# Kernel tuning notes

Measured on AMD Instinct MI355X. Metric: run time of the kernel, lower is better.

The kernel has to match this reference:

```python
import jax, jax.numpy as jnp
import numpy as np

B, T, C, H, HS = 4, 2048, 1024, 16, 64
EPS = 1e-5


def setup_inputs() -> dict:
    key = jax.random.key(0)
    ks = jax.random.split(key, 16)
    s = lambda k, shp, fan: jax.random.normal(k, shp, jnp.float32) * (fan ** -0.5)
    return {
        "x": jax.random.normal(ks[0], (B, T, C), jnp.float32),
        "wq": s(ks[1], (H, C, HS), C), "bq": jnp.zeros((H, HS), jnp.float32),
        "wk": s(ks[2], (H, C, HS), C), "bk": jnp.zeros((H, HS), jnp.float32),
        "wv": s(ks[3], (H, C, HS), C), "bv": jnp.zeros((H, HS), jnp.float32),
        "wp": s(ks[4], (C, C), C), "bp": jnp.zeros((C,), jnp.float32),
        "w1": s(ks[5], (C, 4 * C), C), "b1": jnp.zeros((4 * C,), jnp.float32),
        "w2": s(ks[6], (4 * C, C), 4 * C), "b2": jnp.zeros((C,), jnp.float32),
        "g1": jnp.ones((C,), jnp.float32), "be1": jnp.zeros((C,), jnp.float32),
        "g2": jnp.ones((C,), jnp.float32), "be2": jnp.zeros((C,), jnp.float32),
    }


def _layernorm(x, g, b):
    mu = jnp.mean(x, axis=-1, keepdims=True)
    var = jnp.mean(jnp.square(x - mu), axis=-1, keepdims=True)
    return (x - mu) * jax.lax.rsqrt(var + EPS) * g + b


def reference(x, wq, bq, wk, bk, wv, bv, wp, bp, w1, b1, w2, b2, g1, be1, g2, be2):
    Bc, Tc, Cc = x.shape
    h = _layernorm(x, g1, be1)
    # per-head projections stacked: [B,H,T,HS]
    q = jnp.einsum('btc,hcd->bhtd', h, wq) + bq[None, :, None, :]
    k = jnp.einsum('btc,hcd->bhtd', h, wk) + bk[None, :, None, :]
    v = jnp.einsum('btc,hcd->bhtd', h, wv) + bv[None, :, None, :]
    # NOTE: source scales by 1/sqrt(n_embd), not 1/sqrt(head_size)
    scores = jnp.einsum('bhtd,bhsd->bhts', q, k) * (Cc ** -0.5)
    causal = jnp.tril(jnp.ones((Tc, Tc), bool))
    scores = jnp.where(causal, scores, -jnp.inf)
    attn = jax.nn.softmax(scores, axis=-1)
    out = jnp.einsum('bhts,bhsd->bhtd', attn, v)
    out = out.transpose(0, 2, 1, 3).reshape(Bc, Tc, Cc)  # concat heads
    x = x + out @ wp + bp
    h2 = _layernorm(x, g2, be2)
    ffn = jax.nn.relu(h2 @ w1 + b1) @ w2 + b2
    return x + ffn
```

## Files before the change

kernel.cpp:

```cpp
#include <hip/hip_runtime.h>


constexpr int Bb = 4, Tt = 2048, Cc = 1024, Hh = 16, HSz = 64, Ff = 4096;
constexpr int Mrows = Bb * Tt;

typedef __attribute__((ext_vector_type(8))) short bf16x8;
typedef __attribute__((ext_vector_type(4))) float f32x4;

__device__ __forceinline__ ushort f2bf(float f) {
  uint u = __builtin_bit_cast(uint, f);
  uint r = (u + 0x7fffu + ((u >> 16) & 1u)) >> 16;
  return (ushort)r;
}
__device__ __forceinline__ float bf2f(ushort s) {
  return __builtin_bit_cast(float, ((uint)s) << 16);
}
__device__ __forceinline__ uint cvtpk_bf16(float lo, float hi) {
  uint r;
  asm("v_cvt_pk_bf16_f32 %0, %1, %2" : "=v"(r) : "v"(lo), "v"(hi));
  return r;
}
__device__ __forceinline__ void gload16(const void* g, void* l) {
  __builtin_amdgcn_global_load_lds(
      (const __attribute__((address_space(1))) void*)g,
      (__attribute__((address_space(3))) void*)l, 16, 0, 0);
}

__global__ __launch_bounds__(256) void ln_kernel(const float* __restrict__ x,
                                                 const float* __restrict__ g,
                                                 const float* __restrict__ b,
                                                 ushort* __restrict__ out) {
  int row = blockIdx.x;
  const float* xr = x + (size_t)row * Cc;
  int c4 = threadIdx.x * 4;
  float4 v = *(const float4*)(xr + c4);
  float s1 = v.x + v.y + v.z + v.w;
  float s2 = v.x * v.x + v.y * v.y + v.z * v.z + v.w * v.w;
#pragma unroll
  for (int off = 32; off >= 1; off >>= 1) {
    s1 += __shfl_xor(s1, off);
    s2 += __shfl_xor(s2, off);
  }
  __shared__ float red[8];
  int wid = threadIdx.x >> 6, lane = threadIdx.x & 63;
  if (lane == 0) { red[wid] = s1; red[4 + wid] = s2; }
  __syncthreads();
  float t1 = red[0] + red[1] + red[2] + red[3];
  float t2 = red[4] + red[5] + red[6] + red[7];
  float mu = t1 * (1.0f / Cc);
  float var = t2 * (1.0f / Cc) - mu * mu;
  float rs = rsqrtf(var + 1e-5f);
  float4 gv = *(const float4*)(g + c4);
  float4 bv = *(const float4*)(b + c4);
  ushort4 o;
  o.x = f2bf((v.x - mu) * rs * gv.x + bv.x);
  o.y = f2bf((v.y - mu) * rs * gv.y + bv.y);
  o.z = f2bf((v.z - mu) * rs * gv.z + bv.z);
  o.w = f2bf((v.w - mu) * rs * gv.w + bv.w);
  *(ushort4*)(out + (size_t)row * Cc + c4) = o;
}

__device__ __forceinline__ void tcast_body(const float* __restrict__ src,
                                           ushort* __restrict__ dst, int ldS,
                                           int ldD, int r0, int c0) {
  __shared__ float t[32][33];
  int c = threadIdx.x & 31, r8 = threadIdx.x >> 5;
#pragma unroll
  for (int i = 0; i < 4; ++i) {
    int r = r8 + i * 8;
    t[r][c] = src[(size_t)(r0 + r) * ldS + c0 + c];
  }
  __syncthreads();
#pragma unroll
  for (int i = 0; i < 4; ++i) {
    int rr = r8 + i * 8;
    dst[(size_t)(c0 + rr) * ldD + r0 + c] = f2bf(t[c][rr]);
  }
}

__global__ __launch_bounds__(256) void tcast_kernel(const float* __restrict__ src,
                                                    ushort* __restrict__ dst,
                                                    int ldS, int ldD) {
  tcast_body(src, dst, ldS, ldD, blockIdx.x * 32, blockIdx.y * 32);
}

__global__ __launch_bounds__(256) void tcast_qkv(const float* __restrict__ wq,
                                                 const float* __restrict__ wk,
                                                 const float* __restrict__ wv,
                                                 ushort* __restrict__ dst) {
  int z = blockIdx.z, zz = z >> 4, h = z & 15;
  const float* src = (zz == 0 ? wq : (zz == 1 ? wk : wv)) + (size_t)h * Cc * HSz;
  ushort* d = dst + (size_t)(zz * 1024 + h * 64) * 1024;
  tcast_body(src, d, HSz, Cc, blockIdx.x * 32, blockIdx.y * 32);
}

__global__ __launch_bounds__(256) void bias_concat(const float* __restrict__ bq,
                                                   const float* __restrict__ bk,
                                                   const float* __restrict__ bv,
                                                   float* __restrict__ dst) {
  int i = blockIdx.x * 256 + threadIdx.x;
  dst[i] = i < 1024 ? bq[i] : (i < 2048 ? bk[i - 1024] : bv[i - 2048]);
}

__device__ __forceinline__ void gemm_main(const ushort* __restrict__ A, int lda,
                                          const ushort* __restrict__ Bt, int ldb,
                                          int K, int m0, int n0,
                                          ushort* __restrict__ As,
                                          ushort* __restrict__ Bs,
                                          f32x4 (&acc)[4][2]) {
  int tid = threadIdx.x, wid = tid >> 6, lane = tid & 63;
  int wr = wid >> 2, wc = wid & 3, fr = lane & 15, fq = lane >> 4;
  const ushort* Ag = A + (size_t)m0 * lda;
  const ushort* Bg = Bt + (size_t)n0 * ldb;
  for (int k0 = 0; k0 < K; k0 += 64) {
#pragma unroll
    for (int c = 0; c < 2; ++c) {
      int slot = c * 512 + tid;
      int row = slot >> 3, s = slot & 7;
      int sw = (s << 3) ^ ((row & 7) << 3);
      gload16(Ag + (size_t)row * lda + k0 + sw, As + (size_t)(c * 512 + wid * 64) * 8);
      gload16(Bg + (size_t)row * ldb + k0 + sw, Bs + (size_t)(c * 512 + wid * 64) * 8);
    }
    __syncthreads();
    bf16x8 av[4][2], bv[2][2];
#pragma unroll
    for (int m = 0; m < 4; ++m) {
      int row = wr * 64 + m * 16 + fr;
#pragma unroll
      for (int ks = 0; ks < 2; ++ks)
        av[m][ks] = *(const bf16x8*)&As[row * 64 + (((ks * 4 + fq) ^ (row & 7)) << 3)];
    }
#pragma unroll
    for (int n = 0; n < 2; ++n) {
      int row = wc * 32 + n * 16 + fr;
#pragma unroll
      for (int ks = 0; ks < 2; ++ks)
        bv[n][ks] = *(const bf16x8*)&Bs[row * 64 + (((ks * 4 + fq) ^ (row & 7)) << 3)];
    }
#pragma unroll
    for (int m = 0; m < 4; ++m)
#pragma unroll
      for (int n = 0; n < 2; ++n)
#pragma unroll
        for (int ks = 0; ks < 2; ++ks)
          acc[m][n] = __builtin_amdgcn_mfma_f32_16x16x32_bf16(
              av[m][ks], bv[n][ks], acc[m][n], 0, 0, 0);
    __syncthreads();
  }
}

__device__ __forceinline__ void xcd_swz(int& bx, int& by) {
  int bid = blockIdx.x + blockIdx.y * gridDim.x;
  int cpx = (gridDim.x * gridDim.y) >> 3;
  int id = (bid & 7) * cpx + (bid >> 3);
  bx = id % gridDim.x;
  by = id / gridDim.x;
}

template <bool RELU, bool HASRES, bool OUTBF16>
__global__ __launch_bounds__(512) void gemm_bf16(
    const ushort* __restrict__ A, int lda, const ushort* __restrict__ Bt,
    int ldb, const float* __restrict__ bias, const float* __restrict__ res,
    void* __restrict__ Cout, int ldc, int K) {
  __shared__ __align__(16) ushort As[128 * 64];
  __shared__ __align__(16) ushort Bs[128 * 64];
  f32x4 acc[4][2] = {};
  int bx, by;
  xcd_swz(bx, by);
  int m0 = by * 128, n0 = bx * 128;
  gemm_main(A, lda, Bt, ldb, K, m0, n0, As, Bs, acc);
  int lane = threadIdx.x & 63, wid = threadIdx.x >> 6;
  int wr = wid >> 2, wc = wid & 3, fr = lane & 15, fq = lane >> 4;
#pragma unroll
  for (int m = 0; m < 4; ++m) {
    int gm = m0 + wr * 64 + m * 16 + fq * 4;
#pragma unroll
    for (int n = 0; n < 2; ++n) {
      int gn = n0 + wc * 32 + n * 16 + fr;
      float bsv = bias[gn];
#pragma unroll
      for (int j = 0; j < 4; ++j) {
        int row = gm + j;
        float v = acc[m][n][j] + bsv;
        if constexpr (HASRES) v += res[(size_t)row * ldc + gn];
        if constexpr (RELU) v = fmaxf(v, 0.f);
        if constexpr (OUTBF16)
          ((ushort*)Cout)[(size_t)row * ldc + gn] = f2bf(v);
        else
          ((float*)Cout)[(size_t)row * ldc + gn] = v;
      }
    }
  }
}

__global__ __launch_bounds__(512) void gemm_qkv(const ushort* __restrict__ A,
                                                const ushort* __restrict__ Bt,
                                                const float* __restrict__ bias,
                                                ushort* __restrict__ q,
                                                ushort* __restrict__ k,
                                                ushort* __restrict__ vt) {
  __shared__ __align__(16) ushort As[128 * 64];
  __shared__ __align__(16) ushort Bs[128 * 64];
  f32x4 acc[4][2] = {};
  int bx, by;
  xcd_swz(bx, by);
  int m0 = by * 128, n0 = bx * 128;
  gemm_main(A, 1024, Bt, 1024, 1024, m0, n0, As, Bs, acc);
  int lane = threadIdx.x & 63, wid = threadIdx.x >> 6;
  int wr = wid >> 2, wc = wid & 3, fr = lane & 15, fq = lane >> 4;
  const float qscale = 1.4426950408889634f / 32.0f;
#pragma unroll
  for (int m = 0; m < 4; ++m) {
    int gm = m0 + wr * 64 + m * 16 + fq * 4;
#pragma unroll
    for (int n = 0; n < 2; ++n) {
      int gn = n0 + wc * 32 + n * 16 + fr;
      float bsv = bias[gn];
      if (gn < 1024) {
#pragma unroll
        for (int j = 0; j < 4; ++j)
          q[(size_t)(gm + j) * 1024 + gn] = f2bf((acc[m][n][j] + bsv) * qscale);
      } else if (gn < 2048) {
        int col = gn - 1024;
#pragma unroll
        for (int j = 0; j < 4; ++j)
          k[(size_t)(gm + j) * 1024 + col] = f2bf(acc[m][n][j] + bsv);
      } else {
        int dd = gn - 2048, h = dd >> 6, d = dd & 63;
        int bbr = gm >> 11, t = gm & 2047;
        ushort4 pw = {f2bf(acc[m][n][0] + bsv), f2bf(acc[m][n][1] + bsv),
                      f2bf(acc[m][n][2] + bsv), f2bf(acc[m][n][3] + bsv)};
        *(ushort4*)&vt[(((size_t)(bbr * 16 + h)) * 64 + d) * 2048 + t] = pw;
      }
    }
  }
}

constexpr int QB = 128, KVB = 64;
__global__ __launch_bounds__(512) void attn_kernel(const ushort* __restrict__ Qb,
                                                   const ushort* __restrict__ Kb,
                                                   const ushort* __restrict__ Vt,
                                                   ushort* __restrict__ att) {
  __shared__ __align__(16) ushort Klds[64 * 64];
  __shared__ __align__(16) ushort Vlds[64 * 64];
  __shared__ __align__(16) ushort Plds[8][16 * 64];
  int tid = threadIdx.x, wid = tid >> 6, lane = tid & 63;
  int fr = lane & 15, fq = lane >> 4;
  int bh = blockIdx.y, bb = bh >> 4, hh = bh & 15;
  const ushort* qkbase = Qb + ((size_t)bb * Tt) * Cc + hh * HSz;
  const ushort* Kbase = Kb + ((size_t)bb * Tt) * Cc + hh * HSz;
  const ushort* Vbase = Vt + ((size_t)(bb * Hh + hh)) * HSz * Tt;

#pragma unroll 1
  for (int pass = 0; pass < 2; ++pass) {
    int qt = pass ? (Tt / QB - 1 - (int)blockIdx.x) : (int)blockIdx.x;
    int q0 = qt * QB;
    int q0w = q0 + wid * 16;

    bf16x8 Qreg[2];
#pragma unroll
    for (int d2 = 0; d2 < 2; ++d2)
      Qreg[d2] = *(const bf16x8*)(qkbase + (size_t)(q0w + fr) * Cc + d2 * 32 + fq * 8);
    f32x4 Oa[4] = {};
    float mrow = -1e30f, lrow = 0.f;
    int nt = q0 / KVB + 2;

    for (int kt = 0; kt < nt; ++kt) {
      int t0 = kt * KVB;
      __syncthreads();
      {
        int row = tid >> 3;
        int b = (tid & 7) * 16;
        int sw = (b >> 1) ^ ((row & 7) << 3);
        gload16(Kbase + (size_t)(t0 + row) * Cc + sw, (char*)Klds + wid * 1024);
        gload16(Vbase + (size_t)row * Tt + t0 + sw, (char*)Vlds + wid * 1024);
      }
      __syncthreads();
      if (q0w + 15 < t0) continue;

      bf16x8 kf[4][2];
#pragma unroll
      for (int ks = 0; ks < 4; ++ks)
#pragma unroll
        for (int d2 = 0; d2 < 2; ++d2) {
          int row = ks * 16 + fr;
          int off = (d2 * 64 + fq * 16) ^ ((row & 7) << 4);
          kf[ks][d2] = *(const bf16x8*)((const char*)Klds + row * 128 + off);
        }
      f32x4 accs[4] = {};
      __builtin_amdgcn_s_setprio(1);
#pragma unroll
      for (int ks = 0; ks < 4; ++ks) {
        accs[ks] = __builtin_amdgcn_mfma_f32_16x16x32_bf16(
            kf[ks][0], Qreg[0], accs[ks], 0, 0, 0);
        accs[ks] = __builtin_amdgcn_mfma_f32_16x16x32_bf16(
            kf[ks][1], Qreg[1], accs[ks], 0, 0, 0);
      }
      __builtin_amdgcn_s_setprio(0);

      float sv[4][4];
      float vmax = -1e30f;
      if (t0 + 63 <= q0w) {
#pragma unroll
        for (int ks = 0; ks < 4; ++ks)
#pragma unroll
          for (int j = 0; j < 4; ++j) {
            sv[ks][j] = accs[ks][j];
            vmax = fmaxf(vmax, sv[ks][j]);
          }
      } else {
        int qg = q0w + fr;
#pragma unroll
        for (int ks = 0; ks < 4; ++ks)
#pragma unroll
          for (int j = 0; j < 4; ++j) {
            int kg = t0 + ks * 16 + fq * 4 + j;
            float s = accs[ks][j];
            s = (kg <= qg) ? s : -1e30f;
            sv[ks][j] = s;
            vmax = fmaxf(vmax, s);
          }
      }
      vmax = fmaxf(vmax, __shfl_xor(vmax, 16));
      vmax = fmaxf(vmax, __shfl_xor(vmax, 32));
      float mnew = mrow;
      if (!__all(vmax <= mnew + 11.0f)) {
        mnew = fmaxf(mrow, vmax);
        float sf = exp2f(mrow - mnew);
        mrow = mnew;
        lrow *= sf;
#pragma unroll
        for (int j = 0; j < 4; ++j) {
          float sfo = __shfl(sf, fq * 4 + j);
#pragma unroll
          for (int ds = 0; ds < 4; ++ds) Oa[ds][j] *= sfo;
        }
      }
      float ls = 0.f;
      char* pbase = (char*)Plds[wid] + fr * 128;
#pragma unroll
      for (int ks = 0; ks < 4; ++ks) {
        float p0 = exp2f(sv[ks][0] - mnew);
        float p1 = exp2f(sv[ks][1] - mnew);
        float p2 = exp2f(sv[ks][2] - mnew);
        float p3 = exp2f(sv[ks][3] - mnew);
        ls += (p0 + p1) + (p2 + p3);
        uint2 pw = {cvtpk_bf16(p0, p1), cvtpk_bf16(p2, p3)};
        int off = (ks * 32 + fq * 8) ^ ((fr & 7) << 4);
        *(uint2*)(pbase + off) = pw;
      }
      ls += __shfl_xor(ls, 16);
      ls += __shfl_xor(ls, 32);
      lrow += ls;

      bf16x8 vf[4][2];
#pragma unroll
      for (int ds = 0; ds < 4; ++ds)
#pragma unroll
        for (int k2 = 0; k2 < 2; ++k2) {
          int row = ds * 16 + fr;
          int off = (k2 * 64 + fq * 16) ^ ((row & 7) << 4);
          vf[ds][k2] = *(const bf16x8*)((const char*)Vlds + row * 128 + off);
        }
      bf16x8 pf[2];
#pragma unroll
      for (int k2 = 0; k2 < 2; ++k2) {
        int off = (k2 * 64 + fq * 16) ^ ((fr & 7) << 4);
        pf[k2] = *(const bf16x8*)((const char*)Plds[wid] + fr * 128 + off);
      }
      __builtin_amdgcn_s_setprio(1);
#pragma unroll
      for (int ds = 0; ds < 4; ++ds) {
        Oa[ds] = __builtin_amdgcn_mfma_f32_16x16x32_bf16(
            pf[0], vf[ds][0], Oa[ds], 0, 0, 0);
        Oa[ds] = __builtin_amdgcn_mfma_f32_16x16x32_bf16(
            pf[1], vf[ds][1], Oa[ds], 0, 0, 0);
      }
      __builtin_amdgcn_s_setprio(0);
    }

    {
      float linv = 1.f / lrow;
#pragma unroll
      for (int j = 0; j < 4; ++j) {
        float lo = __shfl(linv, fq * 4 + j);
        int qg = q0w + fq * 4 + j;
        ushort* orow = att + (size_t)(bb * Tt + qg) * Cc + hh * HSz;
#pragma unroll
        for (int ds = 0; ds < 4; ++ds)
          orow[ds * 16 + fr] = f2bf(Oa[ds][j] * lo);
      }
    }
  }
}

extern "C" void kernel_launch(void* const* d_in, const int* in_sizes, int n_in,
                              void* d_out, int out_size, void* d_ws,
                              size_t ws_size, hipStream_t stream) {
  const float* x = (const float*)d_in[0];
  const float* wq = (const float*)d_in[1];
  const float* bq = (const float*)d_in[2];
  const float* wk = (const float*)d_in[3];
  const float* bk = (const float*)d_in[4];
  const float* wv = (const float*)d_in[5];
  const float* bv = (const float*)d_in[6];
  const float* wp = (const float*)d_in[7];
  const float* bp = (const float*)d_in[8];
  const float* w1 = (const float*)d_in[9];
  const float* b1 = (const float*)d_in[10];
  const float* w2 = (const float*)d_in[11];
  const float* b2 = (const float*)d_in[12];
  const float* g1 = (const float*)d_in[13];
  const float* be1 = (const float*)d_in[14];
  const float* g2 = (const float*)d_in[15];
  const float* be2 = (const float*)d_in[16];
  float* out = (float*)d_out;

  ushort* Qb = (ushort*)d_ws;
  ushort* Kb = Qb + (size_t)8388608;
  ushort* Vt = Kb + (size_t)8388608;
  ushort* att = Vt + (size_t)8388608;
  ushort* ffh = Qb;
  ushort* h1b = att + (size_t)8388608;
  float* x2 = (float*)(h1b + (size_t)8388608);
  ushort* wqkvT = (ushort*)(x2 + (size_t)8388608);
  ushort* wpT = wqkvT + (size_t)3145728;
  ushort* w1T = wpT + (size_t)1048576;
  ushort* w2T = w1T + (size_t)4194304;
  float* bqkv = (float*)(w2T + (size_t)4194304);

  tcast_qkv<<<dim3(32, 2, 48), 256, 0, stream>>>(wq, wk, wv, wqkvT);
  tcast_kernel<<<dim3(32, 32), 256, 0, stream>>>(wp, wpT, 1024, 1024);
  tcast_kernel<<<dim3(32, 128), 256, 0, stream>>>(w1, w1T, 4096, 1024);
  tcast_kernel<<<dim3(128, 32), 256, 0, stream>>>(w2, w2T, 1024, 4096);
  bias_concat<<<dim3(12), 256, 0, stream>>>(bq, bk, bv, bqkv);

  ln_kernel<<<dim3(Mrows), 256, 0, stream>>>(x, g1, be1, h1b);
  gemm_qkv<<<dim3(24, 64), 512, 0, stream>>>(h1b, wqkvT, bqkv, Qb, Kb, Vt);
  attn_kernel<<<dim3(Tt / QB / 2, Bb * Hh), 512, 0, stream>>>(Qb, Kb, Vt, att);
  gemm_bf16<false, true, false><<<dim3(8, 64), 512, 0, stream>>>(
      att, 1024, wpT, 1024, bp, x, x2, 1024, 1024);
  ln_kernel<<<dim3(Mrows), 256, 0, stream>>>(x2, g2, be2, h1b);
  gemm_bf16<true, false, true><<<dim3(32, 64), 512, 0, stream>>>(
      h1b, 1024, w1T, 1024, b1, nullptr, ffh, 4096, 1024);
  gemm_bf16<false, true, false><<<dim3(8, 64), 512, 0, stream>>>(
      ffh, 4096, w2T, 4096, b2, x2, out, 1024, 4096);
}
```

Baseline: 370.9 us.

## Double-buffer K/V tiles in attention and defer row-sum reductions

```diff
diff --git a/kernel.cpp b/kernel.cpp
--- a/kernel.cpp
+++ b/kernel.cpp
@@ -241,8 +241,8 @@
                                                    const ushort* __restrict__ Kb,
                                                    const ushort* __restrict__ Vt,
                                                    ushort* __restrict__ att) {
-  __shared__ __align__(16) ushort Klds[64 * 64];
-  __shared__ __align__(16) ushort Vlds[64 * 64];
+  __shared__ __align__(16) ushort Klds[2][64 * 64];
+  __shared__ __align__(16) ushort Vlds[2][64 * 64];
   __shared__ __align__(16) ushort Plds[8][16 * 64];
   int tid = threadIdx.x, wid = tid >> 6, lane = tid & 63;
   int fr = lane & 15, fq = lane >> 4;
@@ -250,6 +250,8 @@
   const ushort* qkbase = Qb + ((size_t)bb * Tt) * Cc + hh * HSz;
   const ushort* Kbase = Kb + ((size_t)bb * Tt) * Cc + hh * HSz;
   const ushort* Vbase = Vt + ((size_t)(bb * Hh + hh)) * HSz * Tt;
+  int srow = tid >> 3;
+  int ssw = ((tid & 7) << 3) ^ ((srow & 7) << 3);
 
 #pragma unroll 1
   for (int pass = 0; pass < 2; ++pass) {
@@ -265,19 +267,26 @@
     float mrow = -1e30f, lrow = 0.f;
     int nt = q0 / KVB + 2;
 
+    __syncthreads();
+    gload16(Kbase + (size_t)srow * Cc + ssw, (char*)Klds[0] + wid * 1024);
+    gload16(Vbase + (size_t)srow * Tt + ssw, (char*)Vlds[0] + wid * 1024);
+
+#pragma unroll 1
     for (int kt = 0; kt < nt; ++kt) {
       int t0 = kt * KVB;
+      int c = kt & 1;
       __syncthreads();
-      {
-        int row = tid >> 3;
-        int b = (tid & 7) * 16;
-        int sw = (b >> 1) ^ ((row & 7) << 3);
-        gload16(Kbase + (size_t)(t0 + row) * Cc + sw, (char*)Klds + wid * 1024);
-        gload16(Vbase + (size_t)row * Tt + t0 + sw, (char*)Vlds + wid * 1024);
-      }
-      __syncthreads();
+      if (kt + 1 < nt) {
+        int t0n = t0 + KVB;
+        gload16(Kbase + (size_t)(t0n + srow) * Cc + ssw,
+                (char*)Klds[c ^ 1] + wid * 1024);
+        gload16(Vbase + (size_t)srow * Tt + t0n + ssw,
+                (char*)Vlds[c ^ 1] + wid * 1024);
+      }
       if (q0w + 15 < t0) continue;
 
+      const char* Kc = (const char*)Klds[c];
+      const char* Vc = (const char*)Vlds[c];
       bf16x8 kf[4][2];
 #pragma unroll
       for (int ks = 0; ks < 4; ++ks)
@@ -285,7 +294,7 @@
         for (int d2 = 0; d2 < 2; ++d2) {
           int row = ks * 16 + fr;
           int off = (d2 * 64 + fq * 16) ^ ((row & 7) << 4);
-          kf[ks][d2] = *(const bf16x8*)((const char*)Klds + row * 128 + off);
+          kf[ks][d2] = *(const bf16x8*)(Kc + row * 128 + off);
         }
       f32x4 accs[4] = {};
       __builtin_amdgcn_s_setprio(1);
@@ -321,11 +330,11 @@
             vmax = fmaxf(vmax, s);
           }
       }
-      vmax = fmaxf(vmax, __shfl_xor(vmax, 16));
-      vmax = fmaxf(vmax, __shfl_xor(vmax, 32));
       float mnew = mrow;
-      if (!__all(vmax <= mnew + 11.0f)) {
-        mnew = fmaxf(mrow, vmax);
+      if (!__all(vmax <= mrow + 11.0f)) {
+        float rmax = fmaxf(vmax, __shfl_xor(vmax, 16));
+        rmax = fmaxf(rmax, __shfl_xor(rmax, 32));
+        mnew = fmaxf(mrow, rmax);
         float sf = exp2f(mrow - mnew);
         mrow = mnew;
         lrow *= sf;
@@ -336,7 +345,6 @@
           for (int ds = 0; ds < 4; ++ds) Oa[ds][j] *= sfo;
         }
       }
-      float ls = 0.f;
       char* pbase = (char*)Plds[wid] + fr * 128;
 #pragma unroll
       for (int ks = 0; ks < 4; ++ks) {
@@ -344,14 +352,11 @@
         float p1 = exp2f(sv[ks][1] - mnew);
         float p2 = exp2f(sv[ks][2] - mnew);
         float p3 = exp2f(sv[ks][3] - mnew);
-        ls += (p0 + p1) + (p2 + p3);
+        lrow += (p0 + p1) + (p2 + p3);
         uint2 pw = {cvtpk_bf16(p0, p1), cvtpk_bf16(p2, p3)};
         int off = (ks * 32 + fq * 8) ^ ((fr & 7) << 4);
         *(uint2*)(pbase + off) = pw;
       }
-      ls += __shfl_xor(ls, 16);
-      ls += __shfl_xor(ls, 32);
-      lrow += ls;
 
       bf16x8 vf[4][2];
 #pragma unroll
@@ -360,7 +365,7 @@
         for (int k2 = 0; k2 < 2; ++k2) {
           int row = ds * 16 + fr;
           int off = (k2 * 64 + fq * 16) ^ ((row & 7) << 4);
-          vf[ds][k2] = *(const bf16x8*)((const char*)Vlds + row * 128 + off);
+          vf[ds][k2] = *(const bf16x8*)(Vc + row * 128 + off);
         }
       bf16x8 pf[2];
 #pragma unroll
@@ -380,6 +385,8 @@
     }
 
     {
+      lrow += __shfl_xor(lrow, 16);
+      lrow += __shfl_xor(lrow, 32);
       float linv = 1.f / lrow;
 #pragma unroll
       for (int j = 0; j < 4; ++j) {
```

After: 368.0 us. About the same (-0.8%).
